# Kernel optimization log

Hardware: AMD Instinct MI355X
Metric: run time of the kernel (lower is better)

Reference implementation:

```python
import jax, jax.numpy as jnp
import numpy as np

N_NODES = 100000
N_EDGES = 1600000
NFEAT = 256
NHID = 128
NCLASS = 2
NEG_SLOPE = 0.2


def setup_inputs() -> dict:
    key = jax.random.key(0)
    ks = jax.random.split(key, 8)
    x = jax.random.normal(ks[0], (N_NODES, NFEAT), dtype=jnp.float32)
    edge_index = jax.random.randint(ks[1], (2, N_EDGES), 0, N_NODES, dtype=jnp.int64)
    # GATConv params (heads=1): lin weight (no bias), att_src, att_dst, bias
    W = jax.random.normal(ks[2], (NFEAT, NHID), dtype=jnp.float32) * (1.0 / np.sqrt(NFEAT))
    att_src = jax.random.normal(ks[3], (NHID,), dtype=jnp.float32) * (1.0 / np.sqrt(NHID))
    att_dst = jax.random.normal(ks[4], (NHID,), dtype=jnp.float32) * (1.0 / np.sqrt(NHID))
    bias_gat = jnp.zeros((NHID,), dtype=jnp.float32)
    fc_w = jax.random.normal(ks[5], (NCLASS, NHID), dtype=jnp.float32) * (1.0 / np.sqrt(NHID))
    fc_b = jnp.zeros((NCLASS,), dtype=jnp.float32)
    return {"x": x, "edge_index": edge_index, "W": W, "att_src": att_src,
            "att_dst": att_dst, "bias_gat": bias_gat, "fc_w": fc_w, "fc_b": fc_b}


def reference(x, edge_index, W, att_src, att_dst, bias_gat, fc_w, fc_b):
    N = x.shape[0]
    # add self loops (PyG GATConv default)
    loops = jnp.broadcast_to(jnp.arange(N, dtype=edge_index.dtype)[None, :], (2, N))
    ei = jnp.concatenate([edge_index, loops], axis=1)  # [2, E+N]
    src, dst = ei[0], ei[1]

    h = x @ W                                 # [N, NHID]
    a_src = h @ att_src                       # [N]
    a_dst = h @ att_dst                       # [N]

    e = jax.nn.leaky_relu(a_src[src] + a_dst[dst], NEG_SLOPE)  # [E+N]
    # segment softmax over destination nodes (every node has a self loop)
    m = jax.ops.segment_max(e, dst, num_segments=N)
    ex = jnp.exp(e - m[dst])
    s = jax.ops.segment_sum(ex, dst, num_segments=N)
    alpha = ex / (s[dst] + 1e-16)             # [E+N]

    msg = h[src] * alpha[:, None]             # [E+N, NHID]
    out = jax.ops.segment_sum(msg, dst, num_segments=N) + bias_gat  # [N, NHID]

    logits = out @ fc_w.T + fc_b              # [N, NCLASS]
    return jax.nn.log_softmax(logits, axis=1)
```

## Files before the change

### kernel.cpp

```cpp
#include <hip/hip_runtime.h>
#include <hip/hip_bf16.h>
#include <stdint.h>

#define N_NODES 100000
#define N_EDGES 1600000
#define NFEAT   256
#define NHID    128
#define NEG_SLOPE 0.2f

#define NB_B       1563
#define SLAB       2048
#define BIN_BLOCKS 512

typedef __attribute__((ext_vector_type(8))) short short8;
typedef __attribute__((ext_vector_type(4))) float f32x4;

__device__ __forceinline__ int clamp_node(int v) {
    unsigned u = (unsigned)v;
    return (u < (unsigned)N_NODES) ? (int)u : 0;
}

__device__ __forceinline__ unsigned short f2bf(float f) {
    unsigned u = __float_as_uint(f);
    return (unsigned short)((u + 0x7fffu + ((u >> 16) & 1u)) >> 16);
}
__device__ __forceinline__ unsigned pkbf(float a, float b) {
    __hip_bfloat162 t = __float22bfloat162_rn(make_float2(a, b));
    return *reinterpret_cast<unsigned*>(&t);
}
__device__ __forceinline__ float bflo(unsigned p) { return __uint_as_float(p << 16); }
__device__ __forceinline__ float bfhi(unsigned p) { return __uint_as_float(p & 0xffff0000u); }

__global__ __launch_bounds__(256) void k_conv(
    const float* __restrict__ W, unsigned short* __restrict__ Wt)
{
    int id = blockIdx.x * 256 + threadIdx.x;
    int n = id >> 8, k = id & 255;
    Wt[id] = f2bf(W[k * NHID + n]);
}

#define LDS_STRIDE 40
__global__ __launch_bounds__(256) void k_gemm_mfma(
    const float* __restrict__ x,
    const unsigned short* __restrict__ Wt,
    const float* __restrict__ atts,
    const float* __restrict__ attd,
    unsigned short* __restrict__ hb,
    float* __restrict__ asrc,
    float* __restrict__ adst)
{
    __shared__ unsigned short As[128 * LDS_STRIDE];
    __shared__ unsigned short Bs[128 * LDS_STRIDE];
    __shared__ float satt[128][2];

    const int tid  = threadIdx.x;
    const int wave = tid >> 6;
    const int lane = tid & 63;
    const int wm = wave >> 1, wn = wave & 1;
    const int lr = lane & 15, q = lane >> 4;
    const int blockM = blockIdx.x * 128;

    const int sr = tid >> 1;
    const int hh = tid & 1;

    if (tid < 128) { satt[tid][0] = 0.f; satt[tid][1] = 0.f; }

    f32x4 acc[4][4];
#pragma unroll
    for (int a = 0; a < 4; ++a)
#pragma unroll
        for (int b = 0; b < 4; ++b) acc[a][b] = 0.f;

    const int growA = min(blockM + sr, N_NODES - 1);
    const float* xrow = x + (size_t)growA * NFEAT + hh * 16;
    const unsigned short* wrow = Wt + sr * NFEAT + hh * 16;

    float4 va0, va1, va2, va3;
    uint4  vb0, vb1;
    {
        const float4* xp = (const float4*)xrow;
        va0 = xp[0]; va1 = xp[1]; va2 = xp[2]; va3 = xp[3];
        vb0 = *(const uint4*)(wrow);
        vb1 = *(const uint4*)(wrow + 8);
    }

    for (int kt = 0; kt < 8; ++kt) {
        __syncthreads();
        uint4 pa0 = make_uint4(pkbf(va0.x, va0.y), pkbf(va0.z, va0.w),
                               pkbf(va1.x, va1.y), pkbf(va1.z, va1.w));
        uint4 pa1 = make_uint4(pkbf(va2.x, va2.y), pkbf(va2.z, va2.w),
                               pkbf(va3.x, va3.y), pkbf(va3.z, va3.w));
        *(uint4*)&As[sr * LDS_STRIDE + hh * 16 + 0] = pa0;
        *(uint4*)&As[sr * LDS_STRIDE + hh * 16 + 8] = pa1;
        *(uint4*)&Bs[sr * LDS_STRIDE + hh * 16 + 0] = vb0;
        *(uint4*)&Bs[sr * LDS_STRIDE + hh * 16 + 8] = vb1;
        __syncthreads();

        if (kt < 7) {
            const float4* xp = (const float4*)(xrow + (kt + 1) * 32);
            va0 = xp[0]; va1 = xp[1]; va2 = xp[2]; va3 = xp[3];
            vb0 = *(const uint4*)(wrow + (kt + 1) * 32);
            vb1 = *(const uint4*)(wrow + (kt + 1) * 32 + 8);
        }

        short8 af[4], bfr[4];
#pragma unroll
        for (int mt = 0; mt < 4; ++mt)
            af[mt] = *(const short8*)&As[(wm * 64 + mt * 16 + lr) * LDS_STRIDE + q * 8];
#pragma unroll
        for (int nt = 0; nt < 4; ++nt)
            bfr[nt] = *(const short8*)&Bs[(wn * 64 + nt * 16 + lr) * LDS_STRIDE + q * 8];

#pragma unroll
        for (int mt = 0; mt < 4; ++mt)
#pragma unroll
            for (int nt = 0; nt < 4; ++nt)
                acc[mt][nt] = __builtin_amdgcn_mfma_f32_16x16x32_bf16(
                    af[mt], bfr[nt], acc[mt][nt], 0, 0, 0);
    }

    float attsv[4], attdv[4];
#pragma unroll
    for (int nt = 0; nt < 4; ++nt) {
        attsv[nt] = atts[wn * 64 + nt * 16 + lr];
        attdv[nt] = attd[wn * 64 + nt * 16 + lr];
    }
#pragma unroll
    for (int mt = 0; mt < 4; ++mt) {
#pragma unroll
        for (int reg = 0; reg < 4; ++reg) {
            float s = 0.f, d = 0.f;
#pragma unroll
            for (int nt = 0; nt < 4; ++nt) {
                float v = acc[mt][nt][reg];
                s += v * attsv[nt];
                d += v * attdv[nt];
            }
#pragma unroll
            for (int mask = 8; mask > 0; mask >>= 1) {
                s += __shfl_xor(s, mask);
                d += __shfl_xor(d, mask);
            }
            if (lr == 0) {
                int lrow = wm * 64 + mt * 16 + q * 4 + reg;
                atomicAdd(&satt[lrow][0], s);
                atomicAdd(&satt[lrow][1], d);
            }
        }
    }

#pragma unroll
    for (int mt = 0; mt < 4; ++mt) {
#pragma unroll
        for (int reg = 0; reg < 4; ++reg) {
            int grow = blockM + wm * 64 + mt * 16 + q * 4 + reg;
            if (grow < N_NODES) {
                unsigned short* hp = hb + (size_t)grow * NHID + wn * 64 + lr;
#pragma unroll
                for (int nt = 0; nt < 4; ++nt)
                    hp[nt * 16] = f2bf(acc[mt][nt][reg]);
            }
        }
    }

    __syncthreads();
    if (tid < 128) {
        int g = blockM + tid;
        if (g < N_NODES) {
            asrc[g] = satt[tid][0];
            adst[g] = satt[tid][1];
        }
    }
}

__global__ __launch_bounds__(256) void k_bin(
    const int* __restrict__ ei, int* __restrict__ gcur,
    unsigned* __restrict__ staged)
{
    __shared__ int hist[NB_B];
    __shared__ int base[NB_B];
    const int t = threadIdx.x;
    const int per = (N_EDGES + BIN_BLOCKS - 1) / BIN_BLOCKS;
    const int e0 = blockIdx.x * per;
    const int e1 = min(e0 + per, N_EDGES);

    for (int i = t; i < NB_B; i += 256) hist[i] = 0;
    __syncthreads();
    for (int e = e0 + t; e < e1; e += 256)
        atomicAdd(&hist[clamp_node(ei[N_EDGES + e]) >> 6], 1);
    __syncthreads();
    for (int i = t; i < NB_B; i += 256) {
        int c = hist[i];
        base[i] = c ? atomicAdd(&gcur[i], c) : 0;
        hist[i] = 0;
    }
    __syncthreads();
    for (int e = e0 + t; e < e1; e += 256) {
        int d = clamp_node(ei[N_EDGES + e]);
        int s = clamp_node(ei[e]);
        int b = d >> 6;
        int pos = base[b] + atomicAdd(&hist[b], 1);
        if (pos < SLAB)
            staged[(size_t)b * SLAB + pos] = (unsigned)s | ((unsigned)(d & 63) << 17);
    }
}

__global__ __launch_bounds__(256) void k_sort_agg(
    const unsigned* __restrict__ staged, const int* __restrict__ gcur,
    const float* __restrict__ asrc, const float* __restrict__ adst,
    const unsigned short* __restrict__ hb,
    const float* __restrict__ bias, const float* __restrict__ fcw,
    const float* __restrict__ fcb, float* __restrict__ out)
{
    __shared__ float2 buf[SLAB];
    __shared__ int hist[64], scanv[64], cntv[64];
    __shared__ float asrc_s[64], adst_s[64];

    const int b = blockIdx.x;
    const int t = threadIdx.x;
    const int eb = b * SLAB;
    const int n = min(gcur[b], SLAB);
    const int nodeStart = b * 64;

    if (t < 64) {
        hist[t] = 0;
        int gi = nodeStart + t;
        adst_s[t] = (gi < N_NODES) ? adst[gi] : 0.f;
        asrc_s[t] = (gi < N_NODES) ? asrc[gi] : 0.f;
    }
    __syncthreads();

    for (int j = t; j < n; j += 256)
        atomicAdd(&hist[(staged[eb + j] >> 17) & 63], 1);
    __syncthreads();

    if (t < 64) {
        int v = hist[t];
        int sc = v;
#pragma unroll
        for (int off = 1; off < 64; off <<= 1) {
            int u = __shfl_up(sc, off);
            if (t >= off) sc += u;
        }
        scanv[t] = sc - v;
        cntv[t] = v;
        hist[t] = 0;
    }
    __syncthreads();

    for (int j = t; j < n; j += 256) {
        unsigned pk = staged[eb + j];
        int s  = pk & 0x1FFFF;
        int dl = (pk >> 17) & 63;
        float a = asrc[s] + adst_s[dl];
        a = (a > 0.f) ? a : NEG_SLOPE * a;
        float ew = __expf(fminf(a, 60.f));
        int pos = scanv[dl] + atomicAdd(&hist[dl], 1);
        buf[pos] = make_float2(__int_as_float(s), ew);
    }
    __syncthreads();

    const int wave = t >> 6;
    const int lane = t & 63;
    const unsigned* hrows = (const unsigned*)hb;

    const float b0 = bias[2 * lane], b1 = bias[2 * lane + 1];
    const float w00 = fcw[2 * lane], w01 = fcw[2 * lane + 1];
    const float w10 = fcw[NHID + 2 * lane], w11 = fcw[NHID + 2 * lane + 1];
    const float fb0 = fcb[0], fb1 = fcb[1];

    for (int ln = wave * 16; ln < wave * 16 + 16; ++ln) {
        int i = nodeStart + ln;
        if (i >= N_NODES) break;

        float e0 = asrc_s[ln] + adst_s[ln];
        e0 = (e0 > 0.f) ? e0 : NEG_SLOPE * e0;
        float w = __expf(fminf(e0, 60.f));
        unsigned pself = hrows[(unsigned)i * 64u + lane];
        float accx = w * bflo(pself), accy = w * bfhi(pself), ssum = w;

        const int jb = scanv[ln];
        const int nn = cntv[ln];
        int j = 0;
        for (; j + 8 <= nn; j += 8) {
            float2 m[8];
            unsigned p[8];
#pragma unroll
            for (int u = 0; u < 8; ++u) m[u] = buf[jb + j + u];
#pragma unroll
            for (int u = 0; u < 8; ++u)
                p[u] = hrows[(unsigned)__float_as_int(m[u].x) * 64u + lane];
#pragma unroll
            for (int u = 0; u < 8; ++u) {
                accx += m[u].y * bflo(p[u]);
                accy += m[u].y * bfhi(p[u]);
                ssum += m[u].y;
            }
        }
        for (; j < nn; ++j) {
            float2 m = buf[jb + j];
            unsigned p = hrows[(unsigned)__float_as_int(m.x) * 64u + lane];
            accx += m.y * bflo(p);
            accy += m.y * bfhi(p);
            ssum += m.y;
        }

        float inv = 1.0f / (ssum + 1e-16f);
        float ox = accx * inv + b0;
        float oy = accy * inv + b1;

        float l0 = ox * w00 + oy * w01;
        float l1 = ox * w10 + oy * w11;
#pragma unroll
        for (int off = 32; off > 0; off >>= 1) {
            l0 += __shfl_down(l0, off);
            l1 += __shfl_down(l1, off);
        }
        if (lane == 0) {
            l0 += fb0;
            l1 += fb1;
            float m = fmaxf(l0, l1);
            float ls = m + __logf(__expf(l0 - m) + __expf(l1 - m));
            ((float2*)out)[i] = make_float2(l0 - ls, l1 - ls);
        }
    }
}

extern "C" void kernel_launch(void* const* d_in, const int* in_sizes, int n_in,
                              void* d_out, int out_size, void* d_ws, size_t ws_size,
                              hipStream_t stream)
{
    const float* x    = (const float*)d_in[0];
    const int*   ei   = (const int*)d_in[1];
    const float* W    = (const float*)d_in[2];
    const float* atts = (const float*)d_in[3];
    const float* attd = (const float*)d_in[4];
    const float* bias = (const float*)d_in[5];
    const float* fcw  = (const float*)d_in[6];
    const float* fcb  = (const float*)d_in[7];
    float*       out  = (float*)d_out;

    char* base = (char*)d_ws;
    size_t off = 0;
    auto carve = [&](size_t bytes) -> char* {
        char* p = base + off;
        off = (off + bytes + 255) & ~(size_t)255;
        return p;
    };
    unsigned short* hb     = (unsigned short*)carve((size_t)N_NODES * NHID * 2);
    float*          asrc   = (float*)carve(N_NODES * 4);
    float*          adst   = (float*)carve(N_NODES * 4);
    int*            gcur   = (int*)carve(NB_B * 4);
    unsigned*       staged = (unsigned*)carve((size_t)NB_B * SLAB * 4);
    unsigned short* Wt     = (unsigned short*)carve(NHID * NFEAT * 2);
    (void)ws_size; (void)in_sizes; (void)n_in; (void)out_size;

    hipMemsetAsync(gcur, 0, NB_B * 4, stream);

    const int GB = (N_NODES + 127) / 128;

    k_conv<<<(NHID * NFEAT) / 256, 256, 0, stream>>>(W, Wt);
    k_gemm_mfma<<<GB, 256, 0, stream>>>(x, Wt, atts, attd, hb, asrc, adst);
    k_bin<<<BIN_BLOCKS, 256, 0, stream>>>(ei, gcur, staged);
    k_sort_agg<<<NB_B, 256, 0, stream>>>(staged, gcur, asrc, adst, hb,
                                         bias, fcw, fcb, out);
}
```

Baseline: 311.4 us.

## Shrink GEMM tile to 64 rows with B fragments from global and halve agg buckets

```diff
diff --git a/kernel.cpp b/kernel.cpp
--- a/kernel.cpp
+++ b/kernel.cpp
@@ -8,8 +8,8 @@
 #define NHID    128
 #define NEG_SLOPE 0.2f
 
-#define NB_B       1563
-#define SLAB       2048
+#define NB_B       3125
+#define SLAB       1024
 #define BIN_BLOCKS 512
 
 typedef __attribute__((ext_vector_type(8))) short short8;
@@ -49,74 +49,75 @@
     float* __restrict__ asrc,
     float* __restrict__ adst)
 {
-    __shared__ unsigned short As[128 * LDS_STRIDE];
-    __shared__ unsigned short Bs[128 * LDS_STRIDE];
-    __shared__ float satt[128][2];
+    __shared__ unsigned short As[64 * LDS_STRIDE];
+    __shared__ float satt[64][2];
 
     const int tid  = threadIdx.x;
     const int wave = tid >> 6;
     const int lane = tid & 63;
     const int wm = wave >> 1, wn = wave & 1;
     const int lr = lane & 15, q = lane >> 4;
-    const int blockM = blockIdx.x * 128;
-
-    const int sr = tid >> 1;
-    const int hh = tid & 1;
-
-    if (tid < 128) { satt[tid][0] = 0.f; satt[tid][1] = 0.f; }
-
-    f32x4 acc[4][4];
-#pragma unroll
-    for (int a = 0; a < 4; ++a)
+    const int blockM = blockIdx.x * 64;
+
+    const int ar = tid >> 2;
+    const int aq = tid & 3;
+
+    if (tid < 64) { satt[tid][0] = 0.f; satt[tid][1] = 0.f; }
+
+    f32x4 acc[2][4];
+#pragma unroll
+    for (int a = 0; a < 2; ++a)
 #pragma unroll
         for (int b = 0; b < 4; ++b) acc[a][b] = 0.f;
 
-    const int growA = min(blockM + sr, N_NODES - 1);
-    const float* xrow = x + (size_t)growA * NFEAT + hh * 16;
-    const unsigned short* wrow = Wt + sr * NFEAT + hh * 16;
-
-    float4 va0, va1, va2, va3;
-    uint4  vb0, vb1;
+    const int growA = min(blockM + ar, N_NODES - 1);
+    const float* xrow = x + (size_t)growA * NFEAT + aq * 8;
+
+    const unsigned short* bbase[4];
+#pragma unroll
+    for (int nt = 0; nt < 4; ++nt)
+        bbase[nt] = Wt + (size_t)(wn * 64 + nt * 16 + lr) * NFEAT + q * 8;
+
+    float4 va0, va1;
     {
         const float4* xp = (const float4*)xrow;
-        va0 = xp[0]; va1 = xp[1]; va2 = xp[2]; va3 = xp[3];
-        vb0 = *(const uint4*)(wrow);
-        vb1 = *(const uint4*)(wrow + 8);
-    }
-
+        va0 = xp[0]; va1 = xp[1];
+    }
+    short8 bcur[4], bnxt[4];
+#pragma unroll
+    for (int nt = 0; nt < 4; ++nt)
+        bcur[nt] = *(const short8*)(bbase[nt]);
+
+#pragma unroll
     for (int kt = 0; kt < 8; ++kt) {
         __syncthreads();
-        uint4 pa0 = make_uint4(pkbf(va0.x, va0.y), pkbf(va0.z, va0.w),
-                               pkbf(va1.x, va1.y), pkbf(va1.z, va1.w));
-        uint4 pa1 = make_uint4(pkbf(va2.x, va2.y), pkbf(va2.z, va2.w),
-                               pkbf(va3.x, va3.y), pkbf(va3.z, va3.w));
-        *(uint4*)&As[sr * LDS_STRIDE + hh * 16 + 0] = pa0;
-        *(uint4*)&As[sr * LDS_STRIDE + hh * 16 + 8] = pa1;
-        *(uint4*)&Bs[sr * LDS_STRIDE + hh * 16 + 0] = vb0;
-        *(uint4*)&Bs[sr * LDS_STRIDE + hh * 16 + 8] = vb1;
+        uint4 pa = make_uint4(pkbf(va0.x, va0.y), pkbf(va0.z, va0.w),
+                              pkbf(va1.x, va1.y), pkbf(va1.z, va1.w));
+        *(uint4*)&As[ar * LDS_STRIDE + aq * 8] = pa;
         __syncthreads();
 
         if (kt < 7) {
             const float4* xp = (const float4*)(xrow + (kt + 1) * 32);
-            va0 = xp[0]; va1 = xp[1]; va2 = xp[2]; va3 = xp[3];
-            vb0 = *(const uint4*)(wrow + (kt + 1) * 32);
-            vb1 = *(const uint4*)(wrow + (kt + 1) * 32 + 8);
-        }
-
-        short8 af[4], bfr[4];
-#pragma unroll
-        for (int mt = 0; mt < 4; ++mt)
-            af[mt] = *(const short8*)&As[(wm * 64 + mt * 16 + lr) * LDS_STRIDE + q * 8];
-#pragma unroll
-        for (int nt = 0; nt < 4; ++nt)
-            bfr[nt] = *(const short8*)&Bs[(wn * 64 + nt * 16 + lr) * LDS_STRIDE + q * 8];
-
-#pragma unroll
-        for (int mt = 0; mt < 4; ++mt)
+            va0 = xp[0]; va1 = xp[1];
+#pragma unroll
+            for (int nt = 0; nt < 4; ++nt)
+                bnxt[nt] = *(const short8*)(bbase[nt] + (kt + 1) * 32);
+        }
+
+        short8 af[2];
+#pragma unroll
+        for (int mt = 0; mt < 2; ++mt)
+            af[mt] = *(const short8*)&As[(wm * 32 + mt * 16 + lr) * LDS_STRIDE + q * 8];
+
+#pragma unroll
+        for (int mt = 0; mt < 2; ++mt)
 #pragma unroll
             for (int nt = 0; nt < 4; ++nt)
                 acc[mt][nt] = __builtin_amdgcn_mfma_f32_16x16x32_bf16(
-                    af[mt], bfr[nt], acc[mt][nt], 0, 0, 0);
+                    af[mt], bcur[nt], acc[mt][nt], 0, 0, 0);
+
+#pragma unroll
+        for (int nt = 0; nt < 4; ++nt) bcur[nt] = bnxt[nt];
     }
 
     float attsv[4], attdv[4];
@@ -126,7 +127,7 @@
         attdv[nt] = attd[wn * 64 + nt * 16 + lr];
     }
 #pragma unroll
-    for (int mt = 0; mt < 4; ++mt) {
+    for (int mt = 0; mt < 2; ++mt) {
 #pragma unroll
         for (int reg = 0; reg < 4; ++reg) {
             float s = 0.f, d = 0.f;
@@ -142,7 +143,7 @@
                 d += __shfl_xor(d, mask);
             }
             if (lr == 0) {
-                int lrow = wm * 64 + mt * 16 + q * 4 + reg;
+                int lrow = wm * 32 + mt * 16 + q * 4 + reg;
                 atomicAdd(&satt[lrow][0], s);
                 atomicAdd(&satt[lrow][1], d);
             }
@@ -150,10 +151,10 @@
     }
 
 #pragma unroll
-    for (int mt = 0; mt < 4; ++mt) {
+    for (int mt = 0; mt < 2; ++mt) {
 #pragma unroll
         for (int reg = 0; reg < 4; ++reg) {
-            int grow = blockM + wm * 64 + mt * 16 + q * 4 + reg;
+            int grow = blockM + wm * 32 + mt * 16 + q * 4 + reg;
             if (grow < N_NODES) {
                 unsigned short* hp = hb + (size_t)grow * NHID + wn * 64 + lr;
 #pragma unroll
@@ -164,7 +165,7 @@
     }
 
     __syncthreads();
-    if (tid < 128) {
+    if (tid < 64) {
         int g = blockM + tid;
         if (g < N_NODES) {
             asrc[g] = satt[tid][0];
@@ -187,7 +188,7 @@
     for (int i = t; i < NB_B; i += 256) hist[i] = 0;
     __syncthreads();
     for (int e = e0 + t; e < e1; e += 256)
-        atomicAdd(&hist[clamp_node(ei[N_EDGES + e]) >> 6], 1);
+        atomicAdd(&hist[clamp_node(ei[N_EDGES + e]) >> 5], 1);
     __syncthreads();
     for (int i = t; i < NB_B; i += 256) {
         int c = hist[i];
@@ -198,10 +199,10 @@
     for (int e = e0 + t; e < e1; e += 256) {
         int d = clamp_node(ei[N_EDGES + e]);
         int s = clamp_node(ei[e]);
-        int b = d >> 6;
+        int b = d >> 5;
         int pos = base[b] + atomicAdd(&hist[b], 1);
         if (pos < SLAB)
-            staged[(size_t)b * SLAB + pos] = (unsigned)s | ((unsigned)(d & 63) << 17);
+            staged[(size_t)b * SLAB + pos] = (unsigned)s | ((unsigned)(d & 31) << 17);
     }
 }
 
@@ -213,32 +214,31 @@
     const float* __restrict__ fcb, float* __restrict__ out)
 {
     __shared__ float2 buf[SLAB];
-    __shared__ int hist[64], scanv[64], cntv[64];
-    __shared__ float asrc_s[64], adst_s[64];
+    __shared__ int hist[32], scanv[32], cntv[32];
+    __shared__ float asrc_s[32], adst_s[32];
 
     const int b = blockIdx.x;
     const int t = threadIdx.x;
     const int eb = b * SLAB;
     const int n = min(gcur[b], SLAB);
-    const int nodeStart = b * 64;
-
-    if (t < 64) {
+    const int nodeStart = b * 32;
+
+    if (t < 32) {
         hist[t] = 0;
-        int gi = nodeStart + t;
-        adst_s[t] = (gi < N_NODES) ? adst[gi] : 0.f;
-        asrc_s[t] = (gi < N_NODES) ? asrc[gi] : 0.f;
+        adst_s[t] = adst[nodeStart + t];
+        asrc_s[t] = asrc[nodeStart + t];
     }
     __syncthreads();
 
     for (int j = t; j < n; j += 256)
-        atomicAdd(&hist[(staged[eb + j] >> 17) & 63], 1);
-    __syncthreads();
-
-    if (t < 64) {
+        atomicAdd(&hist[(staged[eb + j] >> 17) & 31], 1);
+    __syncthreads();
+
+    if (t < 32) {
         int v = hist[t];
         int sc = v;
 #pragma unroll
-        for (int off = 1; off < 64; off <<= 1) {
+        for (int off = 1; off < 32; off <<= 1) {
             int u = __shfl_up(sc, off);
             if (t >= off) sc += u;
         }
@@ -251,7 +251,7 @@
     for (int j = t; j < n; j += 256) {
         unsigned pk = staged[eb + j];
         int s  = pk & 0x1FFFF;
-        int dl = (pk >> 17) & 63;
+        int dl = (pk >> 17) & 31;
         float a = asrc[s] + adst_s[dl];
         a = (a > 0.f) ? a : NEG_SLOPE * a;
         float ew = __expf(fminf(a, 60.f));
@@ -269,9 +269,8 @@
     const float w10 = fcw[NHID + 2 * lane], w11 = fcw[NHID + 2 * lane + 1];
     const float fb0 = fcb[0], fb1 = fcb[1];
 
-    for (int ln = wave * 16; ln < wave * 16 + 16; ++ln) {
+    for (int ln = wave * 8; ln < wave * 8 + 8; ++ln) {
         int i = nodeStart + ln;
-        if (i >= N_NODES) break;
 
         float e0 = asrc_s[ln] + adst_s[ln];
         e0 = (e0 > 0.f) ? e0 : NEG_SLOPE * e0;
@@ -357,7 +356,7 @@
 
     hipMemsetAsync(gcur, 0, NB_B * 4, stream);
 
-    const int GB = (N_NODES + 127) / 128;
+    const int GB = (N_NODES + 63) / 64;
 
     k_conv<<<(NHID * NFEAT) / 256, 256, 0, stream>>>(W, Wt);
     k_gemm_mfma<<<GB, 256, 0, stream>>>(x, Wt, atts, attd, hb, asrc, adst);
```

After: 322.0 us. +3.4%, slower.
